# Performance work log

Measured on AMD Instinct MI355X. Metric: run time of the kernel, lower is better.

## Reference

```python
import jax, jax.numpy as jnp
import numpy as np

B = 8          # batch
N = 4096       # num_nodes
DEG = 16       # off-diagonal neighbors per node
F_OUT = 64     # out_node_features
NE_FEAT = 4096 # num_egdes (edge-feature slots in x, unused by the math)
E = N * (DEG + 1)  # edges incl. self loops = 69632


def _edge_list():
    # Deterministic sparse adjacency: node i -> (i+0 .. i+DEG) mod N.
    # offset 0 reproduces the +eye self-loop in the torch module.
    base = np.arange(N, dtype=np.int64)
    src = np.repeat(base, DEG + 1)
    offs = np.tile(np.arange(DEG + 1, dtype=np.int64), N)
    dst = (src + offs) % N
    return src, dst


def setup_inputs() -> dict:
    key = jax.random.key(0)
    k1, k2, k3 = jax.random.split(key, 3)
    x = jax.random.normal(k1, (B, NE_FEAT + N), dtype=jnp.float32)
    W = 0.1 * jax.random.normal(k2, (1, F_OUT), dtype=jnp.float32)
    a = 0.1 * jax.random.normal(k3, (2 * F_OUT, 1), dtype=jnp.float32)
    src, dst = _edge_list()
    return {"x": x, "W": W, "a": a,
            "src": jnp.asarray(src), "dst": jnp.asarray(dst),
            "num_egdes": NE_FEAT}


def reference(x, W, a, src, dst, num_egdes):
    nodes = x[:, num_egdes:, None]                 # [B, N, 1]
    h = nodes @ W                                  # [B, N, F]
    f = W.shape[1]
    # cat(h_src, h_dst) @ a == h_src @ a[:F] + h_dst @ a[F:]
    e = (jnp.einsum('bef,f->be', h[:, src], a[:f, 0])
         + jnp.einsum('bef,f->be', h[:, dst], a[f:, 0]))   # [B, E]
    alpha = jax.nn.leaky_relu(e)                   # slope 0.01, as nn.LeakyReLU
    alpha = jax.nn.softmax(alpha, axis=1)          # global softmax over ALL edges (dim=1)
    n = h.shape[1]
    adj = jnp.zeros((x.shape[0], n, n), dtype=h.dtype).at[:, src, dst].set(alpha)  # [B,N,N]
    h_prime = adj @ h                              # [B, N, F]
    return jax.nn.leaky_relu(h_prime)
```

## Files before the change

### kernel.cpp

```cpp
#include <hip/hip_runtime.h>

#define NNODES 4096
#define ROWLEN 8192
#define NEDGES (NNODES * 17)
#define FOUT 64

__device__ __forceinline__ float lrelu(float v) {
    return v >= 0.f ? v : 0.01f * v;
}

__global__ __launch_bounds__(1024) void gat_alpha_kernel(
    const float* __restrict__ x, const float* __restrict__ W,
    const float* __restrict__ a, float* __restrict__ tval) {
    const int b = blockIdx.x;
    const int t = threadIdx.x;
    const float* __restrict__ y = x + (size_t)b * ROWLEN + NNODES;

    __shared__ float sy[NNODES];
    __shared__ float sm[16], sz[16];

    for (int i = t; i < NNODES; i += 1024) sy[i] = y[i];

    float S1 = 0.f, S2 = 0.f;
    #pragma unroll
    for (int f = 0; f < FOUT; ++f) {
        float w = W[f];
        S1 += w * a[f];
        S2 += w * a[FOUT + f];
    }
    __syncthreads();

    float m = -1e30f, Z = 0.f;
    for (int ei = t; ei < NEDGES; ei += 1024) {
        int i = ei / 17;
        int o = ei - i * 17;
        float v = lrelu(sy[i] * S1 + sy[(i + o) & (NNODES - 1)] * S2);
        if (v > m) { Z = Z * __expf(m - v) + 1.f; m = v; }
        else       { Z += __expf(v - m); }
    }
    #pragma unroll
    for (int s = 1; s < 64; s <<= 1) {
        float mo = __shfl_xor(m, s);
        float Zo = __shfl_xor(Z, s);
        float mn = fmaxf(m, mo);
        Z = Z * __expf(m - mn) + Zo * __expf(mo - mn);
        m = mn;
    }
    int wid = t >> 6, lane = t & 63;
    if (lane == 0) { sm[wid] = m; sz[wid] = Z; }
    __syncthreads();
    if (t == 0) {
        float M = sm[0], ZZ = sz[0];
        #pragma unroll
        for (int w = 1; w < 16; ++w) {
            float mo = sm[w], Zo = sz[w];
            float mn = fmaxf(M, mo);
            ZZ = ZZ * __expf(M - mn) + Zo * __expf(mo - mn);
            M = mn;
        }
        sm[0] = M; sz[0] = ZZ;
    }
    __syncthreads();
    m = sm[0];
    const float invZ = 1.f / sz[0];

    for (int i = t; i < NNODES; i += 1024) {
        float yi = sy[i] * S1;
        float acc = 0.f;
        #pragma unroll
        for (int o = 0; o < 17; ++o) {
            float yd = sy[(i + o) & (NNODES - 1)];
            float v = lrelu(yi + yd * S2);
            acc += __expf(v - m) * yd;
        }
        tval[b * NNODES + i] = acc * invZ;
    }
}

__global__ __launch_bounds__(256) void gat_out_kernel(
    const float* __restrict__ tval, const float* __restrict__ W,
    float* __restrict__ out) {
    const int idx = blockIdx.x * 256 + threadIdx.x;
    const float tv = tval[idx >> 4];
    const float4 w = reinterpret_cast<const float4*>(W)[idx & 15];
    float4 r;
    r.x = lrelu(tv * w.x);
    r.y = lrelu(tv * w.y);
    r.z = lrelu(tv * w.z);
    r.w = lrelu(tv * w.w);
    reinterpret_cast<float4*>(out)[idx] = r;
}

extern "C" void kernel_launch(void* const* d_in, const int* in_sizes, int n_in,
                              void* d_out, int out_size, void* d_ws, size_t ws_size,
                              hipStream_t stream) {
    const float* x = (const float*)d_in[0];
    const float* W = (const float*)d_in[1];
    const float* a = (const float*)d_in[2];
    float* out  = (float*)d_out;
    float* tval = (float*)d_ws;

    gat_alpha_kernel<<<8, 1024, 0, stream>>>(x, W, a, tval);

    const int n4 = 8 * NNODES * FOUT / 4;
    gat_out_kernel<<<n4 / 256, 256, 0, stream>>>(tval, W, out);
}
```

Baseline: 87.39 us.

## Split softmax reduction across many blocks and fuse node aggregation with output

The old alpha kernel ran only 8 blocks, one per batch, so most of the GPU sat idle. Now a first kernel computes partial max and sum-of-exponentials over 68 chunks per batch (544 blocks). A second kernel merges these partials, computes each node's 17-edge weighted sum with 16 lanes per node, and writes the output row directly, removing the intermediate tval pass. The cost is redundant recomputation of the partial merge and of S1/S2 in every block, plus uncached global reads of y instead of shared memory.

Result: faster. 74.06 us (-15.2%).

```diff
diff --git a/kernel.cpp b/kernel.cpp
--- a/kernel.cpp
+++ b/kernel.cpp
@@ -3,23 +3,22 @@
 #define NNODES 4096
 #define ROWLEN 8192
 #define NEDGES (NNODES * 17)
+#define NCHUNK 68
 #define FOUT 64
 
 __device__ __forceinline__ float lrelu(float v) {
     return v >= 0.f ? v : 0.01f * v;
 }
 
-__global__ __launch_bounds__(1024) void gat_alpha_kernel(
+__global__ __launch_bounds__(256) void gat_part(
     const float* __restrict__ x, const float* __restrict__ W,
-    const float* __restrict__ a, float* __restrict__ tval) {
-    const int b = blockIdx.x;
+    const float* __restrict__ a, float* __restrict__ pm,
+    float* __restrict__ pz) {
+    const int blk = blockIdx.x;
+    const int b = blk / NCHUNK;
+    const int c = blk - b * NCHUNK;
     const int t = threadIdx.x;
     const float* __restrict__ y = x + (size_t)b * ROWLEN + NNODES;
-
-    __shared__ float sy[NNODES];
-    __shared__ float sm[16], sz[16];
-
-    for (int i = t; i < NNODES; i += 1024) sy[i] = y[i];
 
     float S1 = 0.f, S2 = 0.f;
     #pragma unroll
@@ -28,67 +27,115 @@
         S1 += w * a[f];
         S2 += w * a[FOUT + f];
     }
-    __syncthreads();
 
-    float m = -1e30f, Z = 0.f;
-    for (int ei = t; ei < NEDGES; ei += 1024) {
+    const int e0 = c * 1024 + t * 4;
+    float v[4];
+    #pragma unroll
+    for (int j = 0; j < 4; ++j) {
+        int ei = e0 + j;
         int i = ei / 17;
         int o = ei - i * 17;
-        float v = lrelu(sy[i] * S1 + sy[(i + o) & (NNODES - 1)] * S2);
-        if (v > m) { Z = Z * __expf(m - v) + 1.f; m = v; }
-        else       { Z += __expf(v - m); }
+        v[j] = lrelu(y[i] * S1 + y[(i + o) & (NNODES - 1)] * S2);
     }
+    float m = fmaxf(fmaxf(v[0], v[1]), fmaxf(v[2], v[3]));
+    float z = 0.f;
+    #pragma unroll
+    for (int j = 0; j < 4; ++j) z += __expf(v[j] - m);
+
     #pragma unroll
     for (int s = 1; s < 64; s <<= 1) {
         float mo = __shfl_xor(m, s);
-        float Zo = __shfl_xor(Z, s);
+        float zo = __shfl_xor(z, s);
         float mn = fmaxf(m, mo);
-        Z = Z * __expf(m - mn) + Zo * __expf(mo - mn);
+        z = z * __expf(m - mn) + zo * __expf(mo - mn);
         m = mn;
     }
-    int wid = t >> 6, lane = t & 63;
-    if (lane == 0) { sm[wid] = m; sz[wid] = Z; }
+    __shared__ float smm[4], szz[4];
+    const int wid = t >> 6, lane = t & 63;
+    if (lane == 0) { smm[wid] = m; szz[wid] = z; }
     __syncthreads();
     if (t == 0) {
-        float M = sm[0], ZZ = sz[0];
+        float M = smm[0], Z = szz[0];
         #pragma unroll
-        for (int w = 1; w < 16; ++w) {
-            float mo = sm[w], Zo = sz[w];
+        for (int w = 1; w < 4; ++w) {
+            float mo = smm[w], zo = szz[w];
             float mn = fmaxf(M, mo);
-            ZZ = ZZ * __expf(M - mn) + Zo * __expf(mo - mn);
+            Z = Z * __expf(M - mn) + zo * __expf(mo - mn);
             M = mn;
         }
-        sm[0] = M; sz[0] = ZZ;
-    }
-    __syncthreads();
-    m = sm[0];
-    const float invZ = 1.f / sz[0];
-
-    for (int i = t; i < NNODES; i += 1024) {
-        float yi = sy[i] * S1;
-        float acc = 0.f;
-        #pragma unroll
-        for (int o = 0; o < 17; ++o) {
-            float yd = sy[(i + o) & (NNODES - 1)];
-            float v = lrelu(yi + yd * S2);
-            acc += __expf(v - m) * yd;
-        }
-        tval[b * NNODES + i] = acc * invZ;
+        pm[blk] = M;
+        pz[blk] = Z;
     }
 }
 
-__global__ __launch_bounds__(256) void gat_out_kernel(
-    const float* __restrict__ tval, const float* __restrict__ W,
-    float* __restrict__ out) {
-    const int idx = blockIdx.x * 256 + threadIdx.x;
-    const float tv = tval[idx >> 4];
-    const float4 w = reinterpret_cast<const float4*>(W)[idx & 15];
+__global__ __launch_bounds__(256) void gat_node(
+    const float* __restrict__ x, const float* __restrict__ W,
+    const float* __restrict__ a, const float* __restrict__ pm,
+    const float* __restrict__ pz, float* __restrict__ out) {
+    const int blk = blockIdx.x;
+    const int b = blk >> 8;
+    const int nbase = (blk & 255) << 4;
+    const int t = threadIdx.x;
+    const float* __restrict__ y = x + (size_t)b * ROWLEN + NNODES;
+
+    float m = -1e30f, z = 0.f;
+    if (t < NCHUNK) { m = pm[b * NCHUNK + t]; z = pz[b * NCHUNK + t]; }
+    #pragma unroll
+    for (int s = 1; s < 64; s <<= 1) {
+        float mo = __shfl_xor(m, s);
+        float zo = __shfl_xor(z, s);
+        float mn = fmaxf(m, mo);
+        z = z * __expf(m - mn) + zo * __expf(mo - mn);
+        m = mn;
+    }
+    __shared__ float smm[4], szz[4];
+    __shared__ float sM, sIZ;
+    const int wid = t >> 6, lane = t & 63;
+    if (lane == 0) { smm[wid] = m; szz[wid] = z; }
+    __syncthreads();
+    if (t == 0) {
+        float M = smm[0], Z = szz[0];
+        #pragma unroll
+        for (int w = 1; w < 4; ++w) {
+            float mo = smm[w], zo = szz[w];
+            float mn = fmaxf(M, mo);
+            Z = Z * __expf(M - mn) + zo * __expf(mo - mn);
+            M = mn;
+        }
+        sM = M;
+        sIZ = 1.f / Z;
+    }
+    __syncthreads();
+    const float M = sM, invZ = sIZ;
+
+    float S1 = 0.f, S2 = 0.f;
+    #pragma unroll
+    for (int f = 0; f < FOUT; ++f) {
+        float w = W[f];
+        S1 += w * a[f];
+        S2 += w * a[FOUT + f];
+    }
+
+    const int n = nbase + (t >> 4);
+    const int l16 = t & 15;
+    const float yi = y[n] * S1;
+    float yd = y[(n + l16) & (NNODES - 1)];
+    float acc = __expf(lrelu(yi + yd * S2) - M) * yd;
+    if (l16 == 0) {
+        float yd2 = y[(n + 16) & (NNODES - 1)];
+        acc += __expf(lrelu(yi + yd2 * S2) - M) * yd2;
+    }
+    #pragma unroll
+    for (int s = 1; s < 16; s <<= 1) acc += __shfl_xor(acc, s, 16);
+    const float tv = acc * invZ;
+
+    const float4 w4 = reinterpret_cast<const float4*>(W)[l16];
     float4 r;
-    r.x = lrelu(tv * w.x);
-    r.y = lrelu(tv * w.y);
-    r.z = lrelu(tv * w.z);
-    r.w = lrelu(tv * w.w);
-    reinterpret_cast<float4*>(out)[idx] = r;
+    r.x = lrelu(tv * w4.x);
+    r.y = lrelu(tv * w4.y);
+    r.z = lrelu(tv * w4.z);
+    r.w = lrelu(tv * w4.w);
+    reinterpret_cast<float4*>(out)[(size_t)(b * NNODES + n) * 16 + l16] = r;
 }
 
 extern "C" void kernel_launch(void* const* d_in, const int* in_sizes, int n_in,
@@ -97,11 +144,10 @@
     const float* x = (const float*)d_in[0];
     const float* W = (const float*)d_in[1];
     const float* a = (const float*)d_in[2];
-    float* out  = (float*)d_out;
-    float* tval = (float*)d_ws;
+    float* out = (float*)d_out;
+    float* pm = (float*)d_ws;
+    float* pz = pm + 8 * NCHUNK;
 
-    gat_alpha_kernel<<<8, 1024, 0, stream>>>(x, W, a, tval);
-
-    const int n4 = 8 * NNODES * FOUT / 4;
-    gat_out_kernel<<<n4 / 256, 256, 0, stream>>>(tval, W, out);
+    gat_part<<<8 * NCHUNK, 256, 0, stream>>>(x, W, a, pm, pz);
+    gat_node<<<8 * 256, 256, 0, stream>>>(x, W, a, pm, pz, out);
 }
```
